# Optimization experiments

Hardware: AMD Instinct MI355X
Metric: run time of the kernel (lower is better)

## Reference

```python
import jax, jax.numpy as jnp
import numpy as np

N_NODES = 100000
N_EDGES = 1600000
IN_CH, HID_CH, OUT_CH = 128, 128, 64


def setup_inputs() -> dict:
    key = jax.random.key(0)
    k_x, k_e, k1, k2, k3 = jax.random.split(key, 5)
    x = jax.random.normal(k_x, (N_NODES, IN_CH), dtype=jnp.float32)
    edge_index = jax.random.randint(k_e, (2, N_EDGES), 0, N_NODES, dtype=jnp.int64)
    # Glorot-ish init for the three GCNConv weight matrices (no bias).
    W1 = jax.random.normal(k1, (IN_CH, HID_CH), dtype=jnp.float32) / np.sqrt(IN_CH)
    W2 = jax.random.normal(k2, (HID_CH, HID_CH), dtype=jnp.float32) / np.sqrt(HID_CH)
    W3 = jax.random.normal(k3, (HID_CH, OUT_CH), dtype=jnp.float32) / np.sqrt(HID_CH)
    return {"x": x, "edge_index": edge_index, "W1": W1, "W2": W2, "W3": W3}


def _gcn_layer(x, src, dst, W):
    # GCNConv(normalize=False, bias=False): transform then sum-aggregate over edges.
    h = x @ W                      # [N, d_out]
    msgs = h[src]                  # [E, d_out] gather from source nodes
    return jax.ops.segment_sum(msgs, dst, num_segments=N_NODES)  # scatter-add to targets


def reference(x, edge_index, W1, W2, W3):
    src, dst = edge_index[0], edge_index[1]  # PyG flow: source_to_target
    h = _gcn_layer(x, src, dst, W1)
    h = _gcn_layer(h, src, dst, W2)
    h = _gcn_layer(h, src, dst, W3)
    return h  # [N, OUT_CH]
```

## Files before the change

kernel.cpp:

```cpp
#include <hip/hip_runtime.h>

#define N_NODES 100000
#define N_EDGES 1600000
#define CAP 48
#define NBUCK 256
#define NPB 391
#define SCAP 8192
#define EPB 4096

typedef unsigned int uint;
typedef unsigned short ushort;


__global__ void __launch_bounds__(256) bin_edges(const int* __restrict__ src,
                                                 const int* __restrict__ dst,
                                                 int* __restrict__ gcur,
                                                 uint2* __restrict__ seg, int E) {
    __shared__ int ecnt[NBUCK];
    __shared__ int base[NBUCK];
    __shared__ int lcur[NBUCK];
    const int t = threadIdx.x;
    ecnt[t] = 0; lcur[t] = 0;
    __syncthreads();
    const int e0 = blockIdx.x * EPB;
#pragma unroll
    for (int k = 0; k < EPB / 256; k++) {
        int i = e0 + k * 256 + t;
        if (i < E) atomicAdd(&ecnt[dst[i] / NPB], 1);
    }
    __syncthreads();
    base[t] = (ecnt[t] > 0) ? atomicAdd(&gcur[t], ecnt[t]) : 0;
    __syncthreads();
#pragma unroll
    for (int k = 0; k < EPB / 256; k++) {
        int i = e0 + k * 256 + t;
        if (i < E) {
            int d = dst[i];
            int b = d / NPB;
            int s = base[b] + atomicAdd(&lcur[b], 1);
            if (s < SCAP) seg[(size_t)b * SCAP + s] = make_uint2((uint)src[i], (uint)d);
        }
    }
}

__global__ void __launch_bounds__(1024) build_csr(const int* __restrict__ gcur,
                                                  const uint2* __restrict__ seg,
                                                  int* __restrict__ col,
                                                  int* __restrict__ cnt, int n) {
    __shared__ int lc[NPB];
    const int b = blockIdx.x;
    const int t = threadIdx.x;
    for (int i = t; i < NPB; i += 1024) lc[i] = 0;
    __syncthreads();
    int m = gcur[b]; if (m > SCAP) m = SCAP;
    const uint2* sg = seg + (size_t)b * SCAP;
    const int node0 = b * NPB;
    for (int i = t; i < m; i += 1024) {
        uint2 e = sg[i];
        int d = (int)e.y;
        int slot = atomicAdd(&lc[d - node0], 1);
        if (slot < CAP) col[(size_t)d * CAP + slot] = (int)e.x;
    }
    __syncthreads();
    for (int i = t; i < NPB; i += 1024) {
        int node = node0 + i;
        if (node < n) cnt[node] = (lc[i] > CAP) ? CAP : lc[i];
    }
}

__device__ __forceinline__ void fma4(float4& c, float s, const float4& w) {
    c.x += s * w.x; c.y += s * w.y; c.z += s * w.z; c.w += s * w.w;
}

__device__ __forceinline__ ushort bf16r(float f) {
    union { float f; uint u; } v; v.f = f;
    return (ushort)((v.u + 0x7fffu + ((v.u >> 16) & 1u)) >> 16);
}

template <int DOUT, typename OutT>
__global__ void __launch_bounds__(256, 3) gemm_tiled(const float* __restrict__ X,
                                                     const float* __restrict__ W,
                                                     OutT* __restrict__ H, int n) {
    __shared__ __align__(16) float Xs[128][36];
    __shared__ __align__(16) float Ws[32][DOUT];
    const int tid  = threadIdx.x;
    const int row0 = blockIdx.x * 128;
    const int rg   = tid >> 4;
    const int cg   = tid & 15;

    float4 acc0[8], acc1[8];
#pragma unroll
    for (int r = 0; r < 8; r++) {
        acc0[r] = make_float4(0.f, 0.f, 0.f, 0.f);
        if (DOUT == 128) acc1[r] = make_float4(0.f, 0.f, 0.f, 0.f);
    }

    const int lr = tid >> 1;
    const int lh = tid & 1;
    int grow = row0 + lr; if (grow > n - 1) grow = n - 1;
    const float* gx_base = X + (size_t)grow * 128 + lh * 16;

    for (int k0 = 0; k0 < 128; k0 += 32) {
        const float* gx = gx_base + k0;
#pragma unroll
        for (int i = 0; i < 4; i++)
            *(float4*)&Xs[lr][lh * 16 + 4 * i] = *(const float4*)(gx + 4 * i);
        const float4* gw = (const float4*)(W + (size_t)k0 * DOUT);
        float4* sw = (float4*)&Ws[0][0];
        constexpr int WL = (32 * DOUT / 4) / 256;
#pragma unroll
        for (int i = 0; i < WL; i++) sw[tid + 256 * i] = gw[tid + 256 * i];
        __syncthreads();

#pragma unroll
        for (int kk = 0; kk < 32; kk += 4) {
            float4 w00 = *(const float4*)&Ws[kk + 0][cg * 4];
            float4 w01 = *(const float4*)&Ws[kk + 1][cg * 4];
            float4 w02 = *(const float4*)&Ws[kk + 2][cg * 4];
            float4 w03 = *(const float4*)&Ws[kk + 3][cg * 4];
            float4 w10, w11, w12, w13;
            if (DOUT == 128) {
                w10 = *(const float4*)&Ws[kk + 0][64 + cg * 4];
                w11 = *(const float4*)&Ws[kk + 1][64 + cg * 4];
                w12 = *(const float4*)&Ws[kk + 2][64 + cg * 4];
                w13 = *(const float4*)&Ws[kk + 3][64 + cg * 4];
            }
#pragma unroll
            for (int r = 0; r < 8; r++) {
                float4 a = *(const float4*)&Xs[rg * 8 + r][kk];
                fma4(acc0[r], a.x, w00);
                fma4(acc0[r], a.y, w01);
                fma4(acc0[r], a.z, w02);
                fma4(acc0[r], a.w, w03);
                if (DOUT == 128) {
                    fma4(acc1[r], a.x, w10);
                    fma4(acc1[r], a.y, w11);
                    fma4(acc1[r], a.z, w12);
                    fma4(acc1[r], a.w, w13);
                }
            }
        }
        __syncthreads();
    }

#pragma unroll
    for (int r = 0; r < 8; r++) {
        int row = row0 + rg * 8 + r;
        if (row < n) {
            if (sizeof(OutT) == 2) {
                ushort4 o0 = make_ushort4(bf16r(acc0[r].x), bf16r(acc0[r].y),
                                          bf16r(acc0[r].z), bf16r(acc0[r].w));
                *(ushort4*)&H[(size_t)row * DOUT + cg * 4] = o0;
                if (DOUT == 128) {
                    ushort4 o1 = make_ushort4(bf16r(acc1[r].x), bf16r(acc1[r].y),
                                              bf16r(acc1[r].z), bf16r(acc1[r].w));
                    *(ushort4*)&H[(size_t)row * DOUT + 64 + cg * 4] = o1;
                }
            } else {
                *(float4*)&H[(size_t)row * DOUT + cg * 4] = *(float4*)&acc0[r];
                if (DOUT == 128)
                    *(float4*)&H[(size_t)row * DOUT + 64 + cg * 4] = *(float4*)&acc1[r];
            }
        }
    }
}

__device__ __forceinline__ float2 bf2f(uint u) {
    union { uint u; float f; } a, b;
    a.u = u << 16; b.u = u & 0xffff0000u;
    return make_float2(a.f, b.f);
}

template <bool FINAL>
__global__ void __launch_bounds__(256) agg64(const uint* __restrict__ T_in,
                                             const int* __restrict__ cnt,
                                             const int* __restrict__ col,
                                             void* __restrict__ T_out, int n) {
    int gid  = blockIdx.x * blockDim.x + threadIdx.x;
    int node = gid >> 5;
    int lane = gid & 31;
    if (node >= n) return;
    int m = cnt[node]; if (m > CAP) m = CAP;
    const int* cb = col + (size_t)node * CAP;
    float2 acc = make_float2(0.f, 0.f);
    int j = 0;
    for (; j + 8 <= m; j += 8) {
        int s0 = cb[j],     s1 = cb[j + 1], s2 = cb[j + 2], s3 = cb[j + 3];
        int s4 = cb[j + 4], s5 = cb[j + 5], s6 = cb[j + 6], s7 = cb[j + 7];
        uint u0 = T_in[(size_t)s0 * 32 + lane];
        uint u1 = T_in[(size_t)s1 * 32 + lane];
        uint u2 = T_in[(size_t)s2 * 32 + lane];
        uint u3 = T_in[(size_t)s3 * 32 + lane];
        uint u4 = T_in[(size_t)s4 * 32 + lane];
        uint u5 = T_in[(size_t)s5 * 32 + lane];
        uint u6 = T_in[(size_t)s6 * 32 + lane];
        uint u7 = T_in[(size_t)s7 * 32 + lane];
        float2 f0 = bf2f(u0), f1 = bf2f(u1), f2 = bf2f(u2), f3 = bf2f(u3);
        float2 f4 = bf2f(u4), f5 = bf2f(u5), f6 = bf2f(u6), f7 = bf2f(u7);
        acc.x += ((f0.x + f1.x) + (f2.x + f3.x)) + ((f4.x + f5.x) + (f6.x + f7.x));
        acc.y += ((f0.y + f1.y) + (f2.y + f3.y)) + ((f4.y + f5.y) + (f6.y + f7.y));
    }
    for (; j + 4 <= m; j += 4) {
        int s0 = cb[j], s1 = cb[j + 1], s2 = cb[j + 2], s3 = cb[j + 3];
        uint u0 = T_in[(size_t)s0 * 32 + lane];
        uint u1 = T_in[(size_t)s1 * 32 + lane];
        uint u2 = T_in[(size_t)s2 * 32 + lane];
        uint u3 = T_in[(size_t)s3 * 32 + lane];
        float2 f0 = bf2f(u0), f1 = bf2f(u1), f2 = bf2f(u2), f3 = bf2f(u3);
        acc.x += (f0.x + f1.x) + (f2.x + f3.x);
        acc.y += (f0.y + f1.y) + (f2.y + f3.y);
    }
    for (; j < m; j++) {
        float2 f = bf2f(T_in[(size_t)cb[j] * 32 + lane]);
        acc.x += f.x; acc.y += f.y;
    }
    if (FINAL) {
        ((float2*)T_out)[(size_t)node * 32 + lane] = acc;
    } else {
        uint o = (uint)bf16r(acc.x) | ((uint)bf16r(acc.y) << 16);
        ((uint*)T_out)[(size_t)node * 32 + lane] = o;
    }
}


static inline size_t align_up(size_t x, size_t a) { return (x + a - 1) & ~(a - 1); }

extern "C" void kernel_launch(void* const* d_in, const int* in_sizes, int n_in,
                              void* d_out, int out_size, void* d_ws, size_t ws_size,
                              hipStream_t stream) {
    const float* x  = (const float*)d_in[0];
    const int*   ei = (const int*)d_in[1];
    const float* W1 = (const float*)d_in[2];
    const float* W2 = (const float*)d_in[3];
    const float* W3 = (const float*)d_in[4];
    float* out = (float*)d_out;

    const int N = N_NODES;
    const int E = N_EDGES;
    const int* src = ei;
    const int* dst = ei + E;

    char* p = (char*)d_ws;
    int*    gcur = (int*)p;   p += align_up((size_t)NBUCK * 4, 256);
    int*    cnt  = (int*)p;   p += align_up((size_t)N * 4, 256);
    uint2*  seg  = (uint2*)p; p += align_up((size_t)NBUCK * SCAP * 8, 256);
    int*    col  = (int*)p;   p += align_up((size_t)N * CAP * 4, 256);
    float*  W23  = (float*)p; p += align_up((size_t)128 * 64 * 4, 256);
    float*  Wc   = (float*)p; p += align_up((size_t)128 * 64 * 4, 256);
    ushort* Y    = (ushort*)p; p += align_up((size_t)N * 64 * 2, 256);
    ushort* Za   = (ushort*)p; p += align_up((size_t)N * 64 * 2, 256);

    hipMemsetAsync(gcur, 0, (size_t)NBUCK * 4, stream);

    gemm_tiled<64, float><<<1, 256, 0, stream>>>(W2, W3, W23, 128);
    gemm_tiled<64, float><<<1, 256, 0, stream>>>(W1, W23, Wc, 128);

    bin_edges<<<(E + EPB - 1) / EPB, 256, 0, stream>>>(src, dst, gcur, seg, E);
    build_csr<<<NBUCK, 1024, 0, stream>>>(gcur, seg, col, cnt, N);

    gemm_tiled<64, ushort><<<(N + 127) / 128, 256, 0, stream>>>(x, Wc, Y, N);

    const int agg_blocks = (N * 32 + 255) / 256;
    agg64<false><<<agg_blocks, 256, 0, stream>>>((const uint*)Y,  cnt, col, Za, N);
    agg64<false><<<agg_blocks, 256, 0, stream>>>((const uint*)Za, cnt, col, Y,  N);
    agg64<true ><<<agg_blocks, 256, 0, stream>>>((const uint*)Y,  cnt, col, out, N);
}
```

Measured before the change: 287.5 us.

## Fuse weight-product GEMMs into binning and CSR build into feature GEMM; widen aggregation lanes

Folds the two tiny weight-product GEMMs into an extra block of the edge-binning kernel, and runs CSR construction and the X·Wc GEMM as disjoint blocks of one launch. This cuts the launch count from seven to five and lets independent work overlap. The aggregation kernel now gives each lane 4 bf16 values (uint2 loads) with 16 lanes per node, so there are fewer threads and wider loads. CSR blocks drop from 1024 to 256 threads, which may slow that phase. Correctness holds because the GEMM reads only Wc, which the previous launch finished writing.

```diff
diff --git a/kernel.cpp b/kernel.cpp
--- a/kernel.cpp
+++ b/kernel.cpp
@@ -11,25 +11,115 @@
 typedef unsigned int uint;
 typedef unsigned short ushort;
 
-
-__global__ void __launch_bounds__(256) bin_edges(const int* __restrict__ src,
-                                                 const int* __restrict__ dst,
-                                                 int* __restrict__ gcur,
-                                                 uint2* __restrict__ seg, int E) {
-    __shared__ int ecnt[NBUCK];
-    __shared__ int base[NBUCK];
-    __shared__ int lcur[NBUCK];
+__device__ __forceinline__ void fma4(float4& c, float s, const float4& w) {
+    c.x += s * w.x; c.y += s * w.y; c.z += s * w.z; c.w += s * w.w;
+}
+
+__device__ __forceinline__ ushort bf16r(float f) {
+    union { float f; uint u; } v; v.f = f;
+    return (ushort)((v.u + 0x7fffu + ((v.u >> 16) & 1u)) >> 16);
+}
+
+struct alignas(16) GemmSmem {
+    float Xs[128][36];
+    float Ws[32][64];
+};
+
+template <typename OutT>
+__device__ __forceinline__ void gemm64_block(GemmSmem& sm, int bid,
+                                             const float* __restrict__ X,
+                                             const float* __restrict__ W,
+                                             OutT* __restrict__ H, int n) {
+    const int tid  = threadIdx.x;
+    const int row0 = bid * 128;
+    const int rg   = tid >> 4;
+    const int cg   = tid & 15;
+
+    float4 acc0[8];
+#pragma unroll
+    for (int r = 0; r < 8; r++) acc0[r] = make_float4(0.f, 0.f, 0.f, 0.f);
+
+    const int lr = tid >> 1;
+    const int lh = tid & 1;
+    int grow = row0 + lr; if (grow > n - 1) grow = n - 1;
+    const float* gx_base = X + (size_t)grow * 128 + lh * 16;
+
+    for (int k0 = 0; k0 < 128; k0 += 32) {
+        const float* gx = gx_base + k0;
+#pragma unroll
+        for (int i = 0; i < 4; i++)
+            *(float4*)&sm.Xs[lr][lh * 16 + 4 * i] = *(const float4*)(gx + 4 * i);
+        const float4* gw = (const float4*)(W + (size_t)k0 * 64);
+        float4* sw = (float4*)&sm.Ws[0][0];
+#pragma unroll
+        for (int i = 0; i < 2; i++) sw[tid + 256 * i] = gw[tid + 256 * i];
+        __syncthreads();
+
+#pragma unroll
+        for (int kk = 0; kk < 32; kk += 4) {
+            float4 w00 = *(const float4*)&sm.Ws[kk + 0][cg * 4];
+            float4 w01 = *(const float4*)&sm.Ws[kk + 1][cg * 4];
+            float4 w02 = *(const float4*)&sm.Ws[kk + 2][cg * 4];
+            float4 w03 = *(const float4*)&sm.Ws[kk + 3][cg * 4];
+#pragma unroll
+            for (int r = 0; r < 8; r++) {
+                float4 a = *(const float4*)&sm.Xs[rg * 8 + r][kk];
+                fma4(acc0[r], a.x, w00);
+                fma4(acc0[r], a.y, w01);
+                fma4(acc0[r], a.z, w02);
+                fma4(acc0[r], a.w, w03);
+            }
+        }
+        __syncthreads();
+    }
+
+#pragma unroll
+    for (int r = 0; r < 8; r++) {
+        int row = row0 + rg * 8 + r;
+        if (row < n) {
+            if constexpr (sizeof(OutT) == 2) {
+                ushort4 o0 = make_ushort4(bf16r(acc0[r].x), bf16r(acc0[r].y),
+                                          bf16r(acc0[r].z), bf16r(acc0[r].w));
+                *(ushort4*)&H[(size_t)row * 64 + cg * 4] = o0;
+            } else {
+                *(float4*)&H[(size_t)row * 64 + cg * 4] = *(float4*)&acc0[r];
+            }
+        }
+    }
+}
+
+union BinWcSmem {
+    struct { int ecnt[NBUCK]; int base[NBUCK]; int lcur[NBUCK]; } b;
+    GemmSmem g;
+};
+
+__global__ void __launch_bounds__(256) bin_wc(const int* __restrict__ src,
+                                              const int* __restrict__ dst,
+                                              int* __restrict__ gcur,
+                                              uint2* __restrict__ seg, int E,
+                                              const float* __restrict__ W1,
+                                              const float* __restrict__ W2,
+                                              const float* __restrict__ W3,
+                                              float* __restrict__ W23,
+                                              float* __restrict__ Wc) {
+    __shared__ BinWcSmem sh;
+    if (blockIdx.x == gridDim.x - 1) {
+        gemm64_block<float>(sh.g, 0, W2, W3, W23, 128);
+        __syncthreads();
+        gemm64_block<float>(sh.g, 0, W1, W23, Wc, 128);
+        return;
+    }
     const int t = threadIdx.x;
-    ecnt[t] = 0; lcur[t] = 0;
+    sh.b.ecnt[t] = 0; sh.b.lcur[t] = 0;
     __syncthreads();
     const int e0 = blockIdx.x * EPB;
 #pragma unroll
     for (int k = 0; k < EPB / 256; k++) {
         int i = e0 + k * 256 + t;
-        if (i < E) atomicAdd(&ecnt[dst[i] / NPB], 1);
+        if (i < E) atomicAdd(&sh.b.ecnt[dst[i] / NPB], 1);
     }
     __syncthreads();
-    base[t] = (ecnt[t] > 0) ? atomicAdd(&gcur[t], ecnt[t]) : 0;
+    sh.b.base[t] = (sh.b.ecnt[t] > 0) ? atomicAdd(&gcur[t], sh.b.ecnt[t]) : 0;
     __syncthreads();
 #pragma unroll
     for (int k = 0; k < EPB / 256; k++) {
@@ -37,131 +127,46 @@
         if (i < E) {
             int d = dst[i];
             int b = d / NPB;
-            int s = base[b] + atomicAdd(&lcur[b], 1);
+            int s = sh.b.base[b] + atomicAdd(&sh.b.lcur[b], 1);
             if (s < SCAP) seg[(size_t)b * SCAP + s] = make_uint2((uint)src[i], (uint)d);
         }
     }
 }
 
-__global__ void __launch_bounds__(1024) build_csr(const int* __restrict__ gcur,
-                                                  const uint2* __restrict__ seg,
-                                                  int* __restrict__ col,
-                                                  int* __restrict__ cnt, int n) {
-    __shared__ int lc[NPB];
-    const int b = blockIdx.x;
-    const int t = threadIdx.x;
-    for (int i = t; i < NPB; i += 1024) lc[i] = 0;
-    __syncthreads();
-    int m = gcur[b]; if (m > SCAP) m = SCAP;
-    const uint2* sg = seg + (size_t)b * SCAP;
-    const int node0 = b * NPB;
-    for (int i = t; i < m; i += 1024) {
-        uint2 e = sg[i];
-        int d = (int)e.y;
-        int slot = atomicAdd(&lc[d - node0], 1);
-        if (slot < CAP) col[(size_t)d * CAP + slot] = (int)e.x;
-    }
-    __syncthreads();
-    for (int i = t; i < NPB; i += 1024) {
-        int node = node0 + i;
-        if (node < n) cnt[node] = (lc[i] > CAP) ? CAP : lc[i];
-    }
-}
-
-__device__ __forceinline__ void fma4(float4& c, float s, const float4& w) {
-    c.x += s * w.x; c.y += s * w.y; c.z += s * w.z; c.w += s * w.w;
-}
-
-__device__ __forceinline__ ushort bf16r(float f) {
-    union { float f; uint u; } v; v.f = f;
-    return (ushort)((v.u + 0x7fffu + ((v.u >> 16) & 1u)) >> 16);
-}
-
-template <int DOUT, typename OutT>
-__global__ void __launch_bounds__(256, 3) gemm_tiled(const float* __restrict__ X,
-                                                     const float* __restrict__ W,
-                                                     OutT* __restrict__ H, int n) {
-    __shared__ __align__(16) float Xs[128][36];
-    __shared__ __align__(16) float Ws[32][DOUT];
-    const int tid  = threadIdx.x;
-    const int row0 = blockIdx.x * 128;
-    const int rg   = tid >> 4;
-    const int cg   = tid & 15;
-
-    float4 acc0[8], acc1[8];
-#pragma unroll
-    for (int r = 0; r < 8; r++) {
-        acc0[r] = make_float4(0.f, 0.f, 0.f, 0.f);
-        if (DOUT == 128) acc1[r] = make_float4(0.f, 0.f, 0.f, 0.f);
-    }
-
-    const int lr = tid >> 1;
-    const int lh = tid & 1;
-    int grow = row0 + lr; if (grow > n - 1) grow = n - 1;
-    const float* gx_base = X + (size_t)grow * 128 + lh * 16;
-
-    for (int k0 = 0; k0 < 128; k0 += 32) {
-        const float* gx = gx_base + k0;
-#pragma unroll
-        for (int i = 0; i < 4; i++)
-            *(float4*)&Xs[lr][lh * 16 + 4 * i] = *(const float4*)(gx + 4 * i);
-        const float4* gw = (const float4*)(W + (size_t)k0 * DOUT);
-        float4* sw = (float4*)&Ws[0][0];
-        constexpr int WL = (32 * DOUT / 4) / 256;
-#pragma unroll
-        for (int i = 0; i < WL; i++) sw[tid + 256 * i] = gw[tid + 256 * i];
-        __syncthreads();
-
-#pragma unroll
-        for (int kk = 0; kk < 32; kk += 4) {
-            float4 w00 = *(const float4*)&Ws[kk + 0][cg * 4];
-            float4 w01 = *(const float4*)&Ws[kk + 1][cg * 4];
-            float4 w02 = *(const float4*)&Ws[kk + 2][cg * 4];
-            float4 w03 = *(const float4*)&Ws[kk + 3][cg * 4];
-            float4 w10, w11, w12, w13;
-            if (DOUT == 128) {
-                w10 = *(const float4*)&Ws[kk + 0][64 + cg * 4];
-                w11 = *(const float4*)&Ws[kk + 1][64 + cg * 4];
-                w12 = *(const float4*)&Ws[kk + 2][64 + cg * 4];
-                w13 = *(const float4*)&Ws[kk + 3][64 + cg * 4];
-            }
-#pragma unroll
-            for (int r = 0; r < 8; r++) {
-                float4 a = *(const float4*)&Xs[rg * 8 + r][kk];
-                fma4(acc0[r], a.x, w00);
-                fma4(acc0[r], a.y, w01);
-                fma4(acc0[r], a.z, w02);
-                fma4(acc0[r], a.w, w03);
-                if (DOUT == 128) {
-                    fma4(acc1[r], a.x, w10);
-                    fma4(acc1[r], a.y, w11);
-                    fma4(acc1[r], a.z, w12);
-                    fma4(acc1[r], a.w, w13);
-                }
-            }
-        }
-        __syncthreads();
-    }
-
-#pragma unroll
-    for (int r = 0; r < 8; r++) {
-        int row = row0 + rg * 8 + r;
-        if (row < n) {
-            if (sizeof(OutT) == 2) {
-                ushort4 o0 = make_ushort4(bf16r(acc0[r].x), bf16r(acc0[r].y),
-                                          bf16r(acc0[r].z), bf16r(acc0[r].w));
-                *(ushort4*)&H[(size_t)row * DOUT + cg * 4] = o0;
-                if (DOUT == 128) {
-                    ushort4 o1 = make_ushort4(bf16r(acc1[r].x), bf16r(acc1[r].y),
-                                              bf16r(acc1[r].z), bf16r(acc1[r].w));
-                    *(ushort4*)&H[(size_t)row * DOUT + 64 + cg * 4] = o1;
-                }
-            } else {
-                *(float4*)&H[(size_t)row * DOUT + cg * 4] = *(float4*)&acc0[r];
-                if (DOUT == 128)
-                    *(float4*)&H[(size_t)row * DOUT + 64 + cg * 4] = *(float4*)&acc1[r];
-            }
-        }
+union CsrGemmSmem {
+    int lc[NPB];
+    GemmSmem g;
+};
+
+__global__ void __launch_bounds__(256, 3) csr_gemm(const int* __restrict__ gcur,
+                                                   const uint2* __restrict__ seg,
+                                                   int* __restrict__ col,
+                                                   int* __restrict__ cnt,
+                                                   const float* __restrict__ X,
+                                                   const float* __restrict__ Wc,
+                                                   ushort* __restrict__ Y, int n) {
+    __shared__ CsrGemmSmem sh;
+    if (blockIdx.x < NBUCK) {
+        const int b = blockIdx.x;
+        const int t = threadIdx.x;
+        for (int i = t; i < NPB; i += 256) sh.lc[i] = 0;
+        __syncthreads();
+        int m = gcur[b]; if (m > SCAP) m = SCAP;
+        const uint2* sg = seg + (size_t)b * SCAP;
+        const int node0 = b * NPB;
+        for (int i = t; i < m; i += 256) {
+            uint2 e = sg[i];
+            int d = (int)e.y;
+            int slot = atomicAdd(&sh.lc[d - node0], 1);
+            if (slot < CAP) col[(size_t)d * CAP + slot] = (int)e.x;
+        }
+        __syncthreads();
+        for (int i = t; i < NPB; i += 256) {
+            int node = node0 + i;
+            if (node < n) cnt[node] = (sh.lc[i] > CAP) ? CAP : sh.lc[i];
+        }
+    } else {
+        gemm64_block<ushort>(sh.g, blockIdx.x - NBUCK, X, Wc, Y, n);
     }
 }
 
@@ -171,54 +176,70 @@
     return make_float2(a.f, b.f);
 }
 
+__device__ __forceinline__ void acc4(float4& acc, uint2 u,
+                                     float2& lo, float2& hi) {
+    lo = bf2f(u.x); hi = bf2f(u.y);
+    (void)acc;
+}
+
 template <bool FINAL>
-__global__ void __launch_bounds__(256) agg64(const uint* __restrict__ T_in,
+__global__ void __launch_bounds__(256) agg64(const uint2* __restrict__ T_in,
                                              const int* __restrict__ cnt,
                                              const int* __restrict__ col,
                                              void* __restrict__ T_out, int n) {
     int gid  = blockIdx.x * blockDim.x + threadIdx.x;
-    int node = gid >> 5;
-    int lane = gid & 31;
+    int node = gid >> 4;
+    int lane = gid & 15;
     if (node >= n) return;
     int m = cnt[node]; if (m > CAP) m = CAP;
     const int* cb = col + (size_t)node * CAP;
-    float2 acc = make_float2(0.f, 0.f);
+    float4 acc = make_float4(0.f, 0.f, 0.f, 0.f);
     int j = 0;
     for (; j + 8 <= m; j += 8) {
         int s0 = cb[j],     s1 = cb[j + 1], s2 = cb[j + 2], s3 = cb[j + 3];
         int s4 = cb[j + 4], s5 = cb[j + 5], s6 = cb[j + 6], s7 = cb[j + 7];
-        uint u0 = T_in[(size_t)s0 * 32 + lane];
-        uint u1 = T_in[(size_t)s1 * 32 + lane];
-        uint u2 = T_in[(size_t)s2 * 32 + lane];
-        uint u3 = T_in[(size_t)s3 * 32 + lane];
-        uint u4 = T_in[(size_t)s4 * 32 + lane];
-        uint u5 = T_in[(size_t)s5 * 32 + lane];
-        uint u6 = T_in[(size_t)s6 * 32 + lane];
-        uint u7 = T_in[(size_t)s7 * 32 + lane];
-        float2 f0 = bf2f(u0), f1 = bf2f(u1), f2 = bf2f(u2), f3 = bf2f(u3);
-        float2 f4 = bf2f(u4), f5 = bf2f(u5), f6 = bf2f(u6), f7 = bf2f(u7);
-        acc.x += ((f0.x + f1.x) + (f2.x + f3.x)) + ((f4.x + f5.x) + (f6.x + f7.x));
-        acc.y += ((f0.y + f1.y) + (f2.y + f3.y)) + ((f4.y + f5.y) + (f6.y + f7.y));
+        uint2 u0 = T_in[(size_t)s0 * 16 + lane];
+        uint2 u1 = T_in[(size_t)s1 * 16 + lane];
+        uint2 u2 = T_in[(size_t)s2 * 16 + lane];
+        uint2 u3 = T_in[(size_t)s3 * 16 + lane];
+        uint2 u4 = T_in[(size_t)s4 * 16 + lane];
+        uint2 u5 = T_in[(size_t)s5 * 16 + lane];
+        uint2 u6 = T_in[(size_t)s6 * 16 + lane];
+        uint2 u7 = T_in[(size_t)s7 * 16 + lane];
+        float2 a0 = bf2f(u0.x), a1 = bf2f(u1.x), a2 = bf2f(u2.x), a3 = bf2f(u3.x);
+        float2 a4 = bf2f(u4.x), a5 = bf2f(u5.x), a6 = bf2f(u6.x), a7 = bf2f(u7.x);
+        float2 b0 = bf2f(u0.y), b1 = bf2f(u1.y), b2 = bf2f(u2.y), b3 = bf2f(u3.y);
+        float2 b4 = bf2f(u4.y), b5 = bf2f(u5.y), b6 = bf2f(u6.y), b7 = bf2f(u7.y);
+        acc.x += ((a0.x + a1.x) + (a2.x + a3.x)) + ((a4.x + a5.x) + (a6.x + a7.x));
+        acc.y += ((a0.y + a1.y) + (a2.y + a3.y)) + ((a4.y + a5.y) + (a6.y + a7.y));
+        acc.z += ((b0.x + b1.x) + (b2.x + b3.x)) + ((b4.x + b5.x) + (b6.x + b7.x));
+        acc.w += ((b0.y + b1.y) + (b2.y + b3.y)) + ((b4.y + b5.y) + (b6.y + b7.y));
     }
     for (; j + 4 <= m; j += 4) {
         int s0 = cb[j], s1 = cb[j + 1], s2 = cb[j + 2], s3 = cb[j + 3];
-        uint u0 = T_in[(size_t)s0 * 32 + lane];
-        uint u1 = T_in[(size_t)s1 * 32 + lane];
-        uint u2 = T_in[(size_t)s2 * 32 + lane];
-        uint u3 = T_in[(size_t)s3 * 32 + lane];
-        float2 f0 = bf2f(u0), f1 = bf2f(u1), f2 = bf2f(u2), f3 = bf2f(u3);
-        acc.x += (f0.x + f1.x) + (f2.x + f3.x);
-        acc.y += (f0.y + f1.y) + (f2.y + f3.y);
+        uint2 u0 = T_in[(size_t)s0 * 16 + lane];
+        uint2 u1 = T_in[(size_t)s1 * 16 + lane];
+        uint2 u2 = T_in[(size_t)s2 * 16 + lane];
+        uint2 u3 = T_in[(size_t)s3 * 16 + lane];
+        float2 a0 = bf2f(u0.x), a1 = bf2f(u1.x), a2 = bf2f(u2.x), a3 = bf2f(u3.x);
+        float2 b0 = bf2f(u0.y), b1 = bf2f(u1.y), b2 = bf2f(u2.y), b3 = bf2f(u3.y);
+        acc.x += (a0.x + a1.x) + (a2.x + a3.x);
+        acc.y += (a0.y + a1.y) + (a2.y + a3.y);
+        acc.z += (b0.x + b1.x) + (b2.x + b3.x);
+        acc.w += (b0.y + b1.y) + (b2.y + b3.y);
     }
     for (; j < m; j++) {
-        float2 f = bf2f(T_in[(size_t)cb[j] * 32 + lane]);
-        acc.x += f.x; acc.y += f.y;
+        uint2 u = T_in[(size_t)cb[j] * 16 + lane];
+        float2 a = bf2f(u.x), b = bf2f(u.y);
+        acc.x += a.x; acc.y += a.y; acc.z += b.x; acc.w += b.y;
     }
     if (FINAL) {
-        ((float2*)T_out)[(size_t)node * 32 + lane] = acc;
+        ((float4*)T_out)[(size_t)node * 16 + lane] = acc;
     } else {
-        uint o = (uint)bf16r(acc.x) | ((uint)bf16r(acc.y) << 16);
-        ((uint*)T_out)[(size_t)node * 32 + lane] = o;
+        uint2 o;
+        o.x = (uint)bf16r(acc.x) | ((uint)bf16r(acc.y) << 16);
+        o.y = (uint)bf16r(acc.z) | ((uint)bf16r(acc.w) << 16);
+        ((uint2*)T_out)[(size_t)node * 16 + lane] = o;
     }
 }
 
@@ -252,16 +273,16 @@
 
     hipMemsetAsync(gcur, 0, (size_t)NBUCK * 4, stream);
 
-    gemm_tiled<64, float><<<1, 256, 0, stream>>>(W2, W3, W23, 128);
-    gemm_tiled<64, float><<<1, 256, 0, stream>>>(W1, W23, Wc, 128);
-
-    bin_edges<<<(E + EPB - 1) / EPB, 256, 0, stream>>>(src, dst, gcur, seg, E);
-    build_csr<<<NBUCK, 1024, 0, stream>>>(gcur, seg, col, cnt, N);
-
-    gemm_tiled<64, ushort><<<(N + 127) / 128, 256, 0, stream>>>(x, Wc, Y, N);
-
-    const int agg_blocks = (N * 32 + 255) / 256;
-    agg64<false><<<agg_blocks, 256, 0, stream>>>((const uint*)Y,  cnt, col, Za, N);
-    agg64<false><<<agg_blocks, 256, 0, stream>>>((const uint*)Za, cnt, col, Y,  N);
-    agg64<true ><<<agg_blocks, 256, 0, stream>>>((const uint*)Y,  cnt, col, out, N);
-}
+    const int bin_blocks = (E + EPB - 1) / EPB;
+    bin_wc<<<bin_blocks + 1, 256, 0, stream>>>(src, dst, gcur, seg, E,
+                                               W1, W2, W3, W23, Wc);
+
+    const int gemm_blocks = (N + 127) / 128;
+    csr_gemm<<<NBUCK + gemm_blocks, 256, 0, stream>>>(gcur, seg, col, cnt,
+                                                      x, Wc, Y, N);
+
+    const int agg_blocks = (N * 16 + 255) / 256;
+    agg64<false><<<agg_blocks, 256, 0, stream>>>((const uint2*)Y,  cnt, col, Za, N);
+    agg64<false><<<agg_blocks, 256, 0, stream>>>((const uint2*)Za, cnt, col, Y,  N);
+    agg64<true ><<<agg_blocks, 256, 0, stream>>>((const uint2*)Y,  cnt, col, out, N);
+}
```

Measured after the change: 253.2 us. 11.9% less time.
